# Performance work log

Measured on AMD Instinct MI355X. Metric: run time of the kernel, lower is better.

The kernel has to match this reference:

```python
import jax, jax.numpy as jnp
import numpy as np

NUM_HEADS = 8
TOPK = 16


def setup_inputs() -> dict:
    key = jax.random.key(0)
    ks = jax.random.split(key, 13)
    B, C, H, W = 2, 512, 64, 64
    Hu, Wu = H // 2, W // 2
    hd = C // NUM_HEADS
    n = lambda k, shape, s=1.0: jax.random.normal(k, shape, dtype=jnp.float32) * s
    return {
        "x": n(ks[0], (B, C, H, W)),
        "upper_feat": n(ks[1], (B, C, Hu, Wu)),
        "gumbel": jax.random.gumbel(ks[2], (B, NUM_HEADS, Hu * Wu), dtype=jnp.float32),
        # 1x1 convs (Conv2d + folded eval-mode BN => weight matrix + bias)
        "q_w": n(ks[3], (C, C), 0.02), "q_b": n(ks[4], (C,), 0.02),
        "kv_w": n(ks[5], (2 * C, C), 0.02), "kv_b": n(ks[6], (2 * C,), 0.02),
        "proj_w": n(ks[7], (C, C), 0.02), "proj_b": n(ks[8], (C,), 0.02),
        # depthwise 7x7 PE conv (groups = C)
        "pe_w": n(ks[9], (C, 1, 7, 7), 0.02), "pe_b": n(ks[10], (C,), 0.02),
        # gate conv1d kernel_size=1: [head_dim, 2*head_dim]
        "gate_w": n(ks[11], (hd, 2 * hd), 0.02), "gate_b": n(ks[12], (hd,), 0.02),
    }


def reference(x, upper_feat, gumbel, q_w, q_b, kv_w, kv_b, proj_w, proj_b,
              pe_w, pe_b, gate_w, gate_b):
    B, C, H, W = x.shape
    hd = C // NUM_HEADS
    Hu, Wu = upper_feat.shape[2], upper_feat.shape[3]
    N, Nu = H * W, Hu * Wu
    scale = hd ** -0.5

    def conv1x1(t, w, b):
        return jnp.einsum('bchw,oc->bohw', t, w) + b[None, :, None, None]

    # coarse attention: q from x, k/v from upper_feat
    q = conv1x1(x, q_w, q_b).reshape(B, NUM_HEADS, hd, N).transpose(0, 1, 3, 2)          # [B,h,N,d]
    kv = conv1x1(upper_feat, kv_w, kv_b).reshape(B, NUM_HEADS, 2 * hd, Nu).transpose(0, 1, 3, 2)
    k, v = kv[..., :hd], kv[..., hd:]                                                    # [B,h,Nu,d]
    sim = jnp.einsum('bhnd,bhmd->bhnm', q, k) * scale                                    # [B,h,N,Nu]
    attn = jax.nn.softmax(sim, axis=-1)
    coarse = jnp.einsum('bhnm,bhmd->bhnd', attn, v)                                      # [B,h,N,d]

    # fine branch: kv from x, top-k token selection via gumbel-softmax scores
    f_kv = conv1x1(x, kv_w, kv_b).reshape(B, NUM_HEADS, 2 * hd, N).transpose(0, 1, 3, 2)
    f_k, f_v = f_kv[..., :hd], f_kv[..., hd:]                                            # [B,h,N,d]

    # heat: channel-mean of x, adaptive-avg-pooled 2x2 to upper resolution (no grad)
    heat = jax.lax.stop_gradient(
        x.mean(axis=1).reshape(B, Hu, 2, Wu, 2).mean(axis=(2, 4)).reshape(B, Nu))
    global_sim = sim.mean(axis=2) * heat[:, None, :]                                     # [B,h,Nu]
    soft_weights = jax.nn.softmax(global_sim + gumbel, axis=-1)
    _, idx = jax.lax.top_k(soft_weights, TOPK)                                           # [B,h,K]

    # map each selected upper-token to its 2x2 block of x-tokens
    h_idx = (idx // Wu) * 2
    w_idx = (idx % Wu) * 2
    idx_full = jnp.concatenate(
        [(h_idx + dh) * W + (w_idx + dw) for dh in range(2) for dw in range(2)], axis=-1)  # [B,h,4K]

    topk_k = jnp.take_along_axis(f_k, idx_full[..., None], axis=2)                       # [B,h,4K,d]
    topk_v = jnp.take_along_axis(f_v, idx_full[..., None], axis=2)
    fine = jax.nn.softmax(jnp.einsum('bhnd,bhmd->bhnm', q, topk_k) * scale, axis=-1)
    refined = jnp.einsum('bhnm,bhmd->bhnd', fine, topk_v)                                # [B,h,N,d]

    # gated fusion (conv1d kernel_size=1 == per-token linear over 2d channels)
    fusion = jnp.concatenate([coarse, refined], axis=-1)                                 # [B,h,N,2d]
    gate = jax.nn.sigmoid(jnp.einsum('bhnc,oc->bhno', fusion, gate_w) + gate_b)
    out = gate * refined + (1.0 - gate) * coarse                                         # [B,h,N,d]

    x_out = out.transpose(0, 1, 3, 2).reshape(B, C, H, W)

    # positional encoding: depthwise 7x7 conv on v, bilinear upsample to (H,W)
    v_rs = v.transpose(0, 1, 3, 2).reshape(B, C, Hu, Wu)
    v_pe = jax.lax.conv_general_dilated(
        v_rs, pe_w, (1, 1), ((3, 3), (3, 3)), feature_group_count=C,
        dimension_numbers=('NCHW', 'OIHW', 'NCHW')) + pe_b[None, :, None, None]
    v_pe = jax.image.resize(v_pe, (B, C, H, W), method='bilinear')

    return conv1x1(x_out + v_pe, proj_w, proj_b)
```

## Files before the change

kernel.cpp:

```cpp
#include <hip/hip_runtime.h>
#include <hip/hip_bf16.h>
#include <cstdint>

typedef __hip_bfloat16 bf16;
typedef unsigned short u16;
typedef __attribute__((ext_vector_type(8))) short bf16x8;
typedef __attribute__((ext_vector_type(4))) float f32x4;

static __device__ __forceinline__ float bs2f(u16 s) {
  unsigned int u = ((unsigned int)s) << 16;
  float f;
  __builtin_memcpy(&f, &u, 4);
  return f;
}
static __device__ __forceinline__ u16 f2bs(float f) {
  bf16 h = __float2bfloat16(f);
  u16 s;
  __builtin_memcpy(&s, &h, 2);
  return s;
}
static __device__ __forceinline__ float ldf(const void* p, size_t i, int f32) {
  return f32 ? ((const float*)p)[i] : bs2f(((const u16*)p)[i]);
}

// ... 75 lines not shown
  const int f32 = *dtf;
  const int b = blockIdx.z, m0 = blockIdx.x * 128, oo0 = blockIdx.y * 64;
  const int t = threadIdx.x, w = t >> 6, lane = t & 63;
  const int quad = lane >> 4, c = lane & 15;
  __shared__ __align__(16) u16 As[128][72];
  __shared__ __align__(16) u16 Ws[64][72];
  f32x4 acc[2][4];
#pragma unroll
  for (int nt = 0; nt < 2; ++nt)
#pragma unroll
    for (int ot = 0; ot < 4; ++ot) acc[nt][ot] = (f32x4){0.f, 0.f, 0.f, 0.f};
  const u16* Ab = A + (size_t)b * M * 512;
  const int arow = t >> 1, acol = (t & 1) * 32;
  const int wrow = t >> 2, wcol = (t & 3) * 16;

  for (int k0 = 0; k0 < 512; k0 += 64) {
    __syncthreads();
    {
      const u16* ga = Ab + (size_t)(m0 + arow) * 512 + k0 + acol;
      uint4* ad = reinterpret_cast<uint4*>(&As[arow][acol]);
      const uint4* gs = reinterpret_cast<const uint4*>(ga);
      ad[0] = gs[0]; ad[1] = gs[1]; ad[2] = gs[2]; ad[3] = gs[3];
      if (f32) {
        const float* gw = (const float*)W + (size_t)(oo0 + wrow) * 512 + k0 + wcol;
#pragma unroll
        for (int e = 0; e < 16; ++e) Ws[wrow][wcol + e] = f2bs(gw[e]);
      } else {
        const u16* gw = (const u16*)W + (size_t)(oo0 + wrow) * 512 + k0 + wcol;
        *reinterpret_cast<uint4*>(&Ws[wrow][wcol])     = *reinterpret_cast<const uint4*>(gw);
        *reinterpret_cast<uint4*>(&Ws[wrow][wcol + 8]) = *reinterpret_cast<const uint4*>(gw + 8);
      }
    }
    __syncthreads();
#pragma unroll
    for (int ks = 0; ks < 2; ++ks) {
      bf16x8 av[2];
      av[0] = *reinterpret_cast<const bf16x8*>(&As[w * 32 + c][ks * 32 + quad * 8]);
      av[1] = *reinterpret_cast<const bf16x8*>(&As[w * 32 + 16 + c][ks * 32 + quad * 8]);
#pragma unroll
      for (int ot = 0; ot < 4; ++ot) {
        bf16x8 wv = *reinterpret_cast<const bf16x8*>(&Ws[ot * 16 + c][ks * 32 + quad * 8]);
#pragma unroll
        for (int nt = 0; nt < 2; ++nt) {
          if (MODE == 3)
            acc[nt][ot] = __builtin_amdgcn_mfma_f32_16x16x32_bf16(wv, av[nt], acc[nt][ot], 0, 0, 0);
          else
            acc[nt][ot] = __builtin_amdgcn_mfma_f32_16x16x32_bf16(av[nt], wv, acc[nt][ot], 0, 0, 0);
        }
      }
    }
  }

  if (MODE == 0) {
    const int h = oo0 >> 6, bh = b * 8 + h;
#pragma unroll
    for (int ot = 0; ot < 4; ++ot) {
      int o = oo0 + ot * 16 + c;
      int d = o & 63;
      float bv = ldf(bias, o, f32);
      float qs = 0.f;
#pragma unroll
      for (int nt = 0; nt < 2; ++nt)
#pragma unroll
        for (int r = 0; r < 4; ++r) {
          int m = m0 + w * 32 + nt * 16 + quad * 4 + r;
          u16 val = f2bs(acc[nt][ot][r] + bv);
          o0[((size_t)bh * M + m) * 64 + d] = val;
          qs += bs2f(val);
        }
      qs += __shfl_xor(qs, 16, 64);
      qs += __shfl_xor(qs, 32, 64);
      if (quad == 0) atomicAdd(&qsum[bh * 64 + d], qs);
    }
  } else {
#pragma unroll
    for (int ot = 0; ot < 4; ++ot)
#pragma unroll
      for (int r = 0; r < 4; ++r) {
        int o = oo0 + ot * 16 + quad * 4 + r;
        float bv = ldf(bias, o, f32);
#pragma unroll
        for (int nt = 0; nt < 2; ++nt) {
          int m = m0 + w * 32 + nt * 16 + c;
          float val = acc[nt][ot][r] + bv;
          size_t oi_ = ((size_t)(b * 512 + o)) * M + m;
          if (f32) ((float*)ob)[oi_] = val;
          else     ((u16*)ob)[oi_] = f2bs(val);
        }
      }
  }
}

__global__ __launch_bounds__(256) void gemm_kv(
    const u16* __restrict__ A, const void* __restrict__ W,
    const void* __restrict__ bias, u16* __restrict__ kb, u16* __restrict__ vTb,
    int M, const int* __restrict__ dtf) {
  const int f32 = *dtf;
  const int b = blockIdx.z, m0 = blockIdx.x * 64, oo0 = blockIdx.y * 64;
  const int t = threadIdx.x, w = t >> 6, lane = t & 63;
  const int quad = lane >> 4, c = lane & 15;
  __shared__ __align__(16) u16 As[64][72];
  __shared__ __align__(16) u16 Ws[64][72];
  f32x4 acc[4];
#pragma unroll
  for (int ot = 0; ot < 4; ++ot) acc[ot] = (f32x4){0.f, 0.f, 0.f, 0.f};
  const u16* Ab = A + (size_t)b * M * 512;
  const int srow = t >> 2, scol = (t & 3) * 16;

  for (int k0 = 0; k0 < 512; k0 += 64) {
    __syncthreads();
    {
      const u16* ga = Ab + (size_t)(m0 + srow) * 512 + k0 + scol;
      *reinterpret_cast<uint4*>(&As[srow][scol])     = *reinterpret_cast<const uint4*>(ga);
      *reinterpret_cast<uint4*>(&As[srow][scol + 8]) = *reinterpret_cast<const uint4*>(ga + 8);
      if (f32) {
        const float* gw = (const float*)W + (size_t)(oo0 + srow) * 512 + k0 + scol;
#pragma unroll
        for (int e = 0; e < 16; ++e) Ws[srow][scol + e] = f2bs(gw[e]);
      } else {
        const u16* gw = (const u16*)W + (size_t)(oo0 + srow) * 512 + k0 + scol;
        *reinterpret_cast<uint4*>(&Ws[srow][scol])     = *reinterpret_cast<const uint4*>(gw);
        *reinterpret_cast<uint4*>(&Ws[srow][scol + 8]) = *reinterpret_cast<const uint4*>(gw + 8);
      }
    }
    __syncthreads();
#pragma unroll
    for (int ks = 0; ks < 2; ++ks) {
      bf16x8 av = *reinterpret_cast<const bf16x8*>(&As[w * 16 + c][ks * 32 + quad * 8]);
#pragma unroll
      for (int ot = 0; ot < 4; ++ot) {
        bf16x8 wv = *reinterpret_cast<const bf16x8*>(&Ws[ot * 16 + c][ks * 32 + quad * 8]);
        acc[ot] = __builtin_amdgcn_mfma_f32_16x16x32_bf16(av, wv, acc[ot], 0, 0, 0);
      }
    }
  }

#pragma unroll
  for (int ot = 0; ot < 4; ++ot) {
    int o = oo0 + ot * 16 + c;
    float bv = ldf(bias, o, f32);
    int hh = o >> 7, jj = o & 127;
#pragma unroll
    for (int r = 0; r < 4; ++r) {
      int m = m0 + w * 16 + quad * 4 + r;
      u16 val = f2bs(acc[ot][r] + bv);
      if (jj < 64) kb[((size_t)(b * 8 + hh) * M + m) * 64 + jj] = val;
      else         vTb[((size_t)(b * 8 + hh) * 64 + (jj & 63)) * M + m] = val;
    }
  }
}

__global__ __launch_bounds__(256) void topk_kernel(
    const float* __restrict__ qsum, const u16* __restrict__ k,
    const float* __restrict__ heat, const void* __restrict__ gumbel,
    int* __restrict__ posb, const int* __restrict__ dtf) {
  const int f32 = *dtf;
  int bh = blockIdx.x, b = bh >> 3, t = threadIdx.x;
  __shared__ float qs[64];
  __shared__ float s[1024];
  __shared__ float rv[256];
  __shared__ int   ri[256];
  if (t < 64) qs[t] = qsum[bh * 64 + t];
  __syncthreads();
  for (int j = 0; j < 4; ++j) {
    int m = t + j * 256;
    const u16* kr = k + ((size_t)bh * 1024 + m) * 64;
    float dot = 0.f;
    for (int d = 0; d < 64; ++d) dot += qs[d] * bs2f(kr[d]);
    s[m] = dot * (0.125f / 4096.0f) * (heat[b * 1024 + m] * (1.0f / 2048.0f)) +
           ldf(gumbel, (size_t)bh * 1024 + m, f32);
  }
  __syncthreads();
  for (int it = 0; it < 16; ++it) {
    float bv = -1e30f; int bi = 0x7fffffff;
    for (int j = 0; j < 4; ++j) {
      int m = t + j * 256; float vv = s[m];
      if (vv > bv || (vv == bv && m < bi)) { bv = vv; bi = m; }
    }
    rv[t] = bv; ri[t] = bi; __syncthreads();
    for (int off = 128; off; off >>= 1) {
      if (t < off) {
        if (rv[t + off] > rv[t] || (rv[t + off] == rv[t] && ri[t + off] < ri[t])) {
          rv[t] = rv[t + off]; ri[t] = ri[t + off];
        }
      }
      __syncthreads();
    }
    if (t == 0) {
      int mi = ri[0]; s[mi] = -1e30f;
      int hy = (mi >> 5) * 2, wx = (mi & 31) * 2;
      posb[bh * 64 + it]      = hy * 64 + wx;
      posb[bh * 64 + 16 + it] = hy * 64 + wx + 1;
      posb[bh * 64 + 32 + it] = (hy + 1) * 64 + wx;
      posb[bh * 64 + 48 + it] = (hy + 1) * 64 + wx + 1;
    }
    __syncthreads();
  }
}

__global__ __launch_bounds__(256) void gather_kv_mfma(
    const u16* __restrict__ xT, const void* __restrict__ kv_w,
    const void* __restrict__ kv_b, const int* __restrict__ posb,
    u16* __restrict__ tkb, u16* __restrict__ tvTb,
    const int* __restrict__ dtf) {
  const int f32 = *dtf;
  const int bh = blockIdx.x, b = bh >> 3, h = bh & 7;
  const int half = blockIdx.y;
  const int t = threadIdx.x, w = t >> 6, lane = t & 63;
  const int quad = lane >> 4, c = lane & 15;
  __shared__ int pos[64];
  __shared__ __align__(16) u16 As[64][72];
  __shared__ __align__(16) u16 Ws[64][72];
  if (t < 64) pos[t] = posb[bh * 64 + t];
  __syncthreads();
  const int obase = h * 128 + half * 64;
  const int srow = t >> 2, scol = (t & 3) * 16;
  const int arow = pos[srow];
  f32x4 acc[4];
#pragma unroll
  for (int ot = 0; ot < 4; ++ot) acc[ot] = (f32x4){0.f, 0.f, 0.f, 0.f};

  for (int k0 = 0; k0 < 512; k0 += 64) {
    __syncthreads();
    {
      const u16* ga = xT + ((size_t)b * 4096 + arow) * 512 + k0 + scol;
      *reinterpret_cast<uint4*>(&As[srow][scol])     = *reinterpret_cast<const uint4*>(ga);
      *reinterpret_cast<uint4*>(&As[srow][scol + 8]) = *reinterpret_cast<const uint4*>(ga + 8);
      if (f32) {
        const float* gw = (const float*)kv_w + (size_t)(obase + srow) * 512 + k0 + scol;
#pragma unroll
        for (int e = 0; e < 16; ++e) Ws[srow][scol + e] = f2bs(gw[e]);
      } else {
        const u16* gw = (const u16*)kv_w + (size_t)(obase + srow) * 512 + k0 + scol;
        *reinterpret_cast<uint4*>(&Ws[srow][scol])     = *reinterpret_cast<const uint4*>(gw);
        *reinterpret_cast<uint4*>(&Ws[srow][scol + 8]) = *reinterpret_cast<const uint4*>(gw + 8);
      }
    }
    __syncthreads();
#pragma unroll
    for (int ks = 0; ks < 2; ++ks) {
      bf16x8 av = *reinterpret_cast<const bf16x8*>(&As[w * 16 + c][ks * 32 + quad * 8]);
#pragma unroll
      for (int ot = 0; ot < 4; ++ot) {
        bf16x8 wv = *reinterpret_cast<const bf16x8*>(&Ws[ot * 16 + c][ks * 32 + quad * 8]);
        acc[ot] = __builtin_amdgcn_mfma_f32_16x16x32_bf16(av, wv, acc[ot], 0, 0, 0);
      }
    }
  }

#pragma unroll
  for (int ot = 0; ot < 4; ++ot) {
    int d = ot * 16 + c;
    float bv = ldf(kv_b, obase + d, f32);
#pragma unroll
    for (int r = 0; r < 4; ++r) {
      int m = w * 16 + quad * 4 + r;
      u16 val = f2bs(acc[ot][r] + bv);
      if (half) tvTb[((size_t)bh * 64 + d) * 64 + m] = val;
      else      tkb[((size_t)bh * 64 + m) * 64 + d] = val;
    }
  }
}

__global__ __launch_bounds__(256) void dwconv_kernel(
    const u16* __restrict__ vT, const void* __restrict__ pe_w,
    const void* __restrict__ pe_b, u16* __restrict__ vpe,
    const int* __restrict__ dtf) {
  const int f32 = *dtf;
  int bc = blockIdx.x;
  int b = bc >> 9, c = bc & 511;
  int h = c >> 6, d = c & 63;
  int t = threadIdx.x;
  __shared__ float img[1024];
  __shared__ float wts[49];
  const u16* base = vT + ((size_t)(b * 8 + h) * 64 + d) * 1024;
  if (t < 128) {
    uint4 v4 = reinterpret_cast<const uint4*>(base)[t];
    u16 tmp[8];
    *reinterpret_cast<uint4*>(tmp) = v4;
#pragma unroll
    for (int e = 0; e < 8; ++e) img[t * 8 + e] = bs2f(tmp[e]);
  }
  if (t < 49) wts[t] = ldf(pe_w, c * 49 + t, f32);
  float bias = ldf(pe_b, c, f32);
  __syncthreads();
  for (int i = t; i < 1024; i += 256) {
    int y = i >> 5, xx = i & 31;
    float a = 0.f;
#pragma unroll
    for (int ky = 0; ky < 7; ++ky) {
      int yy = y + ky - 3;
      if ((unsigned)yy >= 32u) continue;
#pragma unroll
      for (int kx = 0; kx < 7; ++kx) {
        int xc = xx + kx - 3;
        if ((unsigned)xc >= 32u) continue;
        a += img[yy * 32 + xc] * wts[ky * 7 + kx];
      }
    }
    vpe[(size_t)bc * 1024 + i] = f2bs(a + bias);
  }
}

__global__ __launch_bounds__(256) void attn_fused(
    const u16* __restrict__ q, const u16* __restrict__ k,
    const u16* __restrict__ vT, const u16* __restrict__ tkb,
    const u16* __restrict__ tvTb, const u16* __restrict__ gwb,
    const float* __restrict__ gbf, const u16* __restrict__ vpe,
    u16* __restrict__ xsT) {
  const int bh = blockIdx.y, b = bh >> 3, h = bh & 7;
  const int bx = blockIdx.x;
  const int n0 = bx * 128;
  const int t = threadIdx.x, w = t >> 6, lane = t & 63;
  const int quad = lane >> 4, c = lane & 15;

  __shared__ __align__(16) u16 lds[27648];
  u16* Ks = lds;
  u16* Vt = lds + 9216;
  u16* Ps = lds + 18432;

  bf16x8 bq[2][2];
#pragma unroll
  for (int nt = 0; nt < 2; ++nt) {
    const u16* qr = q + ((size_t)bh * 4096 + n0 + w * 32 + nt * 16 + c) * 64;
    bq[nt][0] = *reinterpret_cast<const bf16x8*>(qr + quad * 8);
    bq[nt][1] = *reinterpret_cast<const bf16x8*>(qr + 32 + quad * 8);
  }
  f32x4 po[2][4];
#pragma unroll
  for (int nt = 0; nt < 2; ++nt)
#pragma unroll
    for (int dt = 0; dt < 4; ++dt) po[nt][dt] = (f32x4){0.f, 0.f, 0.f, 0.f};
  float sume[2] = {0.f, 0.f};

  const u16* kbase = k + (size_t)bh * 65536;
  const u16* vbase = vT + (size_t)bh * 65536;
  const int srow = t >> 2, scol = (t & 3) * 16;

  uint4 kr0, kr1, vr0, vr1;
  {
    const u16* gk = kbase + (size_t)srow * 64 + scol;
    kr0 = *reinterpret_cast<const uint4*>(gk);
    kr1 = *reinterpret_cast<const uint4*>(gk + 8);
    const u16* gv = vbase + (size_t)srow * 1024 + scol;
    vr0 = *reinterpret_cast<const uint4*>(gv);
    vr1 = *reinterpret_cast<const uint4*>(gv + 8);
    *reinterpret_cast<uint4*>(&Ks[srow * 72 + scol])     = kr0;
    *reinterpret_cast<uint4*>(&Ks[srow * 72 + scol + 8]) = kr1;
    *reinterpret_cast<uint4*>(&Vt[srow * 72 + scol])     = vr0;
    *reinterpret_cast<uint4*>(&Vt[srow * 72 + scol + 8]) = vr1;
  }

  for (int ch = 0; ch < 16; ++ch) {
    __syncthreads();
    const int buf = ch & 1;
    if (ch + 1 < 16) {
      int m1 = (ch + 1) * 64;
      const u16* gk = kbase + (size_t)(m1 + srow) * 64 + scol;
      kr0 = *reinterpret_cast<const uint4*>(gk);
      kr1 = *reinterpret_cast<const uint4*>(gk + 8);
      const u16* gv = vbase + (size_t)srow * 1024 + m1 + scol;
      vr0 = *reinterpret_cast<const uint4*>(gv);
      vr1 = *reinterpret_cast<const uint4*>(gv + 8);
    }

    f32x4 st[2][4];
#pragma unroll
    for (int mt = 0; mt < 4; ++mt) {
      const u16* krow = &Ks[(buf * 64 + mt * 16 + c) * 72];
      bf16x8 ak0 = *reinterpret_cast<const bf16x8*>(krow + quad * 8);
      bf16x8 ak1 = *reinterpret_cast<const bf16x8*>(krow + 32 + quad * 8);
#pragma unroll
      for (int nt = 0; nt < 2; ++nt) {
        f32x4 acc = (f32x4){0.f, 0.f, 0.f, 0.f};
        acc = __builtin_amdgcn_mfma_f32_16x16x32_bf16(ak0, bq[nt][0], acc, 0, 0, 0);
        acc = __builtin_amdgcn_mfma_f32_16x16x32_bf16(ak1, bq[nt][1], acc, 0, 0, 0);
        st[nt][mt] = acc;
      }
    }
#pragma unroll
    for (int nt = 0; nt < 2; ++nt) {
      float cs = 0.f;
      u16* psw = &Ps[((w * 2 + nt) * 16 + c) * 72];
#pragma unroll
      for (int mt = 0; mt < 4; ++mt) {
        float e0 = __expf(st[nt][mt][0] * 0.125f);
        float e1 = __expf(st[nt][mt][1] * 0.125f);
        float e2 = __expf(st[nt][mt][2] * 0.125f);
        float e3 = __expf(st[nt][mt][3] * 0.125f);
        cs += (e0 + e1) + (e2 + e3);
        ushort4 pw;
        pw.x = f2bs(e0); pw.y = f2bs(e1); pw.z = f2bs(e2); pw.w = f2bs(e3);
        *reinterpret_cast<ushort4*>(psw + mt * 16 + quad * 4) = pw;
      }
      cs += __shfl_xor(cs, 16, 64);
      cs += __shfl_xor(cs, 32, 64);
      sume[nt] += cs;
    }
#pragma unroll
    for (int s = 0; s < 2; ++s) {
      bf16x8 bp0 = *reinterpret_cast<const bf16x8*>(&Ps[((w * 2 + 0) * 16 + c) * 72 + s * 32 + quad * 8]);
      bf16x8 bp1 = *reinterpret_cast<const bf16x8*>(&Ps[((w * 2 + 1) * 16 + c) * 72 + s * 32 + quad * 8]);
#pragma unroll
      for (int dt = 0; dt < 4; ++dt) {
        bf16x8 av = *reinterpret_cast<const bf16x8*>(&Vt[(buf * 64 + dt * 16 + c) * 72 + s * 32 + quad * 8]);
        po[0][dt] = __builtin_amdgcn_mfma_f32_16x16x32_bf16(av, bp0, po[0][dt], 0, 0, 0);
        po[1][dt] = __builtin_amdgcn_mfma_f32_16x16x32_bf16(av, bp1, po[1][dt], 0, 0, 0);
      }
    }

    if (ch + 1 < 16) {
      const int nb = buf ^ 1;
      *reinterpret_cast<uint4*>(&Ks[(nb * 64 + srow) * 72 + scol])     = kr0;
      *reinterpret_cast<uint4*>(&Ks[(nb * 64 + srow) * 72 + scol + 8]) = kr1;
      *reinterpret_cast<uint4*>(&Vt[(nb * 64 + srow) * 72 + scol])     = vr0;
      *reinterpret_cast<uint4*>(&Vt[(nb * 64 + srow) * 72 + scol + 8]) = vr1;
    }
  }

  __syncthreads();
  u16* fus = lds;
  u16* vl  = lds + 17408;
  float* gbl = (float*)(lds + 25088);

  for (int idx = t; idx < 768; idx += 256) {
    int seg = idx & 3, ch2 = (idx >> 2) & 63, r = idx >> 8;
    int vrow = bx - 1 + r;
    vrow = vrow < 0 ? 0 : (vrow > 31 ? 31 : vrow);
    const uint4* src = reinterpret_cast<const uint4*>(
        vpe + ((size_t)(b * 512 + h * 64 + ch2)) * 1024 + vrow * 32);
    *reinterpret_cast<uint4*>(&vl[(r * 64 + ch2) * 40 + seg * 8]) = src[seg];
  }
  if (t < 64) gbl[t] = gbf[t];
  __syncthreads();

  for (int nt = 0; nt < 2; ++nt) {
    u16* fusw = &fus[((w * 2 + nt) * 16 + c) * 136];
    f32x4 st[4];
#pragma unroll
    for (int mt = 0; mt < 4; ++mt) {
      f32x4 acc = (f32x4){0.f, 0.f, 0.f, 0.f};
#pragma unroll
      for (int s = 0; s < 2; ++s) {
        bf16x8 ak = *reinterpret_cast<const bf16x8*>(
            &tkb[((size_t)bh * 64 + mt * 16 + c) * 64 + s * 32 + quad * 8]);
        acc = __builtin_amdgcn_mfma_f32_16x16x32_bf16(ak, bq[nt][s], acc, 0, 0, 0);
      }
      st[mt] = acc;
    }
    float sume2 = 0.f;
#pragma unroll
    for (int mt = 0; mt < 4; ++mt) {
      float e0 = __expf(st[mt][0] * 0.125f);
      float e1 = __expf(st[mt][1] * 0.125f);
      float e2 = __expf(st[mt][2] * 0.125f);
      float e3 = __expf(st[mt][3] * 0.125f);
      sume2 += (e0 + e1) + (e2 + e3);
      ushort4 pw;
      pw.x = f2bs(e0); pw.y = f2bs(e1); pw.z = f2bs(e2); pw.w = f2bs(e3);
      *reinterpret_cast<ushort4*>(fusw + mt * 16 + quad * 4) = pw;
    }
    sume2 += __shfl_xor(sume2, 16, 64);
    sume2 += __shfl_xor(sume2, 32, 64);
    float inv2 = 1.0f / sume2;

    f32x4 po2[4];
#pragma unroll
    for (int dt = 0; dt < 4; ++dt) po2[dt] = (f32x4){0.f, 0.f, 0.f, 0.f};
#pragma unroll
    for (int s = 0; s < 2; ++s) {
      bf16x8 bp = *reinterpret_cast<const bf16x8*>(fusw + s * 32 + quad * 8);
#pragma unroll
      for (int dt = 0; dt < 4; ++dt) {
        bf16x8 av = *reinterpret_cast<const bf16x8*>(
            &tvTb[((size_t)bh * 64 + dt * 16 + c) * 64 + s * 32 + quad * 8]);
        po2[dt] = __builtin_amdgcn_mfma_f32_16x16x32_bf16(av, bp, po2[dt], 0, 0, 0);
      }
    }

    float invc = 1.0f / sume[nt];
#pragma unroll
    for (int dt = 0; dt < 4; ++dt) {
      ushort4 cw, rw;
      cw.x = f2bs(po[nt][dt][0] * invc); cw.y = f2bs(po[nt][dt][1] * invc);
      cw.z = f2bs(po[nt][dt][2] * invc); cw.w = f2bs(po[nt][dt][3] * invc);
      rw.x = f2bs(po2[dt][0] * inv2);    rw.y = f2bs(po2[dt][1] * inv2);
      rw.z = f2bs(po2[dt][2] * inv2);    rw.w = f2bs(po2[dt][3] * inv2);
      *reinterpret_cast<ushort4*>(fusw + dt * 16 + quad * 4)      = cw;
      *reinterpret_cast<ushort4*>(fusw + 64 + dt * 16 + quad * 4) = rw;
    }

    f32x4 ga[4];
#pragma unroll
    for (int ot = 0; ot < 4; ++ot) ga[ot] = (f32x4){0.f, 0.f, 0.f, 0.f};
#pragma unroll
    for (int s = 0; s < 4; ++s) {
      bf16x8 bf = *reinterpret_cast<const bf16x8*>(fusw + s * 32 + quad * 8);
#pragma unroll
      for (int ot = 0; ot < 4; ++ot) {
        bf16x8 ag = *reinterpret_cast<const bf16x8*>(
            gwb + (ot * 16 + c) * 128 + s * 32 + quad * 8);
        ga[ot] = __builtin_amdgcn_mfma_f32_16x16x32_bf16(ag, bf, ga[ot], 0, 0, 0);
      }
    }

    const int ylocal = (w * 32 + nt * 16) >> 6;
    const int x = (w * 32 + nt * 16 + c) & 63;
    float wy0, wy1; int i0, i1;
    if (ylocal == 0) { wy0 = 0.25f; wy1 = 0.75f; i0 = (bx > 0) ? 0 : 1; i1 = 1; }
    else             { wy0 = 0.75f; wy1 = 0.25f; i0 = 1; i1 = (bx < 31) ? 2 : 1; }
    int jx = x >> 1, x0, x1; float wx0, wx1;
    if ((x & 1) == 0) { x0 = (jx > 0) ? jx - 1 : 0; x1 = jx; wx0 = 0.25f; wx1 = 0.75f; }
    else              { x0 = jx; x1 = (jx < 31) ? jx + 1 : 31; wx0 = 0.75f; wx1 = 0.25f; }
#pragma unroll
    for (int dt = 0; dt < 4; ++dt) {
      ushort4 ow;
      u16 tmp[4];
#pragma unroll
      for (int r = 0; r < 4; ++r) {
        int row = dt * 16 + quad * 4 + r;
        float ref = po2[dt][r] * inv2;
        float coar = bs2f(fusw[row]);
        float g = 1.0f / (1.0f + __expf(-(ga[dt][r] + gbl[row])));
        float vv = wy0 * (wx0 * bs2f(vl[(i0 * 64 + row) * 40 + x0]) +
                          wx1 * bs2f(vl[(i0 * 64 + row) * 40 + x1])) +
                   wy1 * (wx0 * bs2f(vl[(i1 * 64 + row) * 40 + x0]) +
                          wx1 * bs2f(vl[(i1 * 64 + row) * 40 + x1]));
        tmp[r] = f2bs(g * ref + (1.0f - g) * coar + vv);
      }
      ow.x = tmp[0]; ow.y = tmp[1]; ow.z = tmp[2]; ow.w = tmp[3];
      *reinterpret_cast<ushort4*>(fusw + dt * 16 + quad * 4) = ow;
    }

    {
      int nl = lane >> 2, cs = (lane & 3) * 16;
      const u16* srcrow = &fus[((w * 2 + nt) * 16 + nl) * 136 + cs];
      u16* dst = xsT + ((size_t)b * 4096 + n0 + w * 32 + nt * 16 + nl) * 512 + h * 64 + cs;
      *reinterpret_cast<uint4*>(dst)     = *reinterpret_cast<const uint4*>(srcrow);
      *reinterpret_cast<uint4*>(dst + 8) = *reinterpret_cast<const uint4*>(srcrow + 8);
    }
  }
}

extern "C" void kernel_launch(void* const* d_in, const int* in_sizes, int n_in,
                              void* d_out, int out_size, void* d_ws, size_t ws_size,
                              hipStream_t stream) {
  const void* x    = d_in[0];
  const void* up   = d_in[1];
  const void* gum  = d_in[2];
  const void* q_w  = d_in[3];
  const void* q_b  = d_in[4];
  const void* kv_w = d_in[5];
  const void* kv_b = d_in[6];
  const void* p_w  = d_in[7];
  const void* p_b  = d_in[8];
  const void* pe_w = d_in[9];
  const void* pe_b = d_in[10];
  const void* g_w  = d_in[11];
  const void* g_b  = d_in[12];

  float* ws    = (float*)d_ws;
  int*   dtf   = (int*)ws;
  float* qsum  = ws + 16;
  float* heat  = qsum + 1024;
  int*   posb  = (int*)(heat + 2048);
  float* gbf   = (float*)(posb + 1024);
  u16*   gwb   = (u16*)(gbf + 64);
  u16*   tkb   = gwb + 8192;
  u16*   tvTb  = tkb + 65536;
  u16*   qb    = tvTb + 65536;
  u16*   kb    = qb + 4194304;
  u16*   vTb   = kb + 1048576;
  u16*   xT    = vTb + 1048576;
  u16*   upT   = xT + 4194304;
  u16*   xsT   = upT + 1048576;
  u16*   vpe   = xsT + 4194304;

  dim3 blk(256);
  hipMemsetAsync(ws, 0, (16 + 1024 + 2048) * 4, stream);
  detect_dtype<<<dim3(64), blk, 0, stream>>>((const uint4*)x, dtf);
  prep_gate<<<dim3(1), blk, 0, stream>>>(g_w, g_b, gwb, gbf, dtf);
  transpose_bf16<<<dim3(64, 8, 2), blk, 0, stream>>>(x, xT, 4096, heat, dtf);
  transpose_bf16<<<dim3(16, 8, 2), blk, 0, stream>>>(up, upT, 1024, nullptr, dtf);
  gemm128<0><<<dim3(32, 8, 2), blk, 0, stream>>>(xT, q_w, q_b, qb, nullptr, qsum, 4096, dtf);
  gemm_kv<<<dim3(16, 16, 2), blk, 0, stream>>>(upT, kv_w, kv_b, kb, vTb, 1024, dtf);
  topk_kernel<<<dim3(16), blk, 0, stream>>>(qsum, kb, heat, gum, posb, dtf);
  gather_kv_mfma<<<dim3(16, 2), blk, 0, stream>>>(xT, kv_w, kv_b, posb, tkb, tvTb, dtf);
  dwconv_kernel<<<dim3(1024), blk, 0, stream>>>(vTb, pe_w, pe_b, vpe, dtf);
  attn_fused<<<dim3(32, 16), blk, 0, stream>>>(qb, kb, vTb, tkb, tvTb, gwb, gbf, vpe, xsT);
  gemm128<3><<<dim3(32, 8, 2), blk, 0, stream>>>(xsT, p_w, p_b, nullptr, d_out, nullptr, 4096, dtf);
}
```

Baseline: 261.7 us.

## Halve attention tile to 64 queries per block and single-buffer K/V

The fused attention kernel now handles 64 query tokens per block instead of 128, one 16-row tile per wave, and the grid doubles to 64x16 blocks. K/V chunks move from a double-buffered LDS ring to a single buffer with an extra barrier per chunk, which halves LDS use and adds a launch-bounds occupancy hint. The aim is more resident blocks and waves per CU to hide latency on 1024 blocks. The costs are re-reading all of K/V once per smaller block and more synchronization stalls, since the prefetched K/V chunk no longer overlaps the MFMA work.

```diff
diff --git a/kernel.cpp b/kernel.cpp
--- a/kernel.cpp
+++ b/kernel.cpp
@@ -401,7 +401,7 @@
   }
 }
 
-__global__ __launch_bounds__(256) void attn_fused(
+__global__ __launch_bounds__(256, 4) void attn_fused(
     const u16* __restrict__ q, const u16* __restrict__ k,
     const u16* __restrict__ vT, const u16* __restrict__ tkb,
     const u16* __restrict__ tvTb, const u16* __restrict__ gwb,
@@ -409,28 +409,25 @@
     u16* __restrict__ xsT) {
   const int bh = blockIdx.y, b = bh >> 3, h = bh & 7;
   const int bx = blockIdx.x;
-  const int n0 = bx * 128;
+  const int n0 = bx * 64;
   const int t = threadIdx.x, w = t >> 6, lane = t & 63;
   const int quad = lane >> 4, c = lane & 15;
 
-  __shared__ __align__(16) u16 lds[27648];
+  __shared__ __align__(16) u16 lds[13824];
   u16* Ks = lds;
-  u16* Vt = lds + 9216;
-  u16* Ps = lds + 18432;
-
-  bf16x8 bq[2][2];
-#pragma unroll
-  for (int nt = 0; nt < 2; ++nt) {
-    const u16* qr = q + ((size_t)bh * 4096 + n0 + w * 32 + nt * 16 + c) * 64;
-    bq[nt][0] = *reinterpret_cast<const bf16x8*>(qr + quad * 8);
-    bq[nt][1] = *reinterpret_cast<const bf16x8*>(qr + 32 + quad * 8);
-  }
-  f32x4 po[2][4];
-#pragma unroll
-  for (int nt = 0; nt < 2; ++nt)
-#pragma unroll
-    for (int dt = 0; dt < 4; ++dt) po[nt][dt] = (f32x4){0.f, 0.f, 0.f, 0.f};
-  float sume[2] = {0.f, 0.f};
+  u16* Vt = lds + 4608;
+  u16* Ps = lds + 9216;
+
+  bf16x8 bq[2];
+  {
+    const u16* qr = q + ((size_t)bh * 4096 + n0 + w * 16 + c) * 64;
+    bq[0] = *reinterpret_cast<const bf16x8*>(qr + quad * 8);
+    bq[1] = *reinterpret_cast<const bf16x8*>(qr + 32 + quad * 8);
+  }
+  f32x4 po[4];
+#pragma unroll
+  for (int dt = 0; dt < 4; ++dt) po[dt] = (f32x4){0.f, 0.f, 0.f, 0.f};
+  float sume = 0.f;
 
   const u16* kbase = k + (size_t)bh * 65536;
   const u16* vbase = vT + (size_t)bh * 65536;
@@ -444,17 +441,17 @@
     const u16* gv = vbase + (size_t)srow * 1024 + scol;
     vr0 = *reinterpret_cast<const uint4*>(gv);
     vr1 = *reinterpret_cast<const uint4*>(gv + 8);
+  }
+
+  for (int ch = 0; ch < 16; ++ch) {
+    __syncthreads();
     *reinterpret_cast<uint4*>(&Ks[srow * 72 + scol])     = kr0;
     *reinterpret_cast<uint4*>(&Ks[srow * 72 + scol + 8]) = kr1;
     *reinterpret_cast<uint4*>(&Vt[srow * 72 + scol])     = vr0;
     *reinterpret_cast<uint4*>(&Vt[srow * 72 + scol + 8]) = vr1;
-  }
-
-  for (int ch = 0; ch < 16; ++ch) {
-    __syncthreads();
-    const int buf = ch & 1;
+    __syncthreads();
     if (ch + 1 < 16) {
-      int m1 = (ch + 1) * 64;
+      const int m1 = (ch + 1) * 64;
       const u16* gk = kbase + (size_t)(m1 + srow) * 64 + scol;
       kr0 = *reinterpret_cast<const uint4*>(gk);
       kr1 = *reinterpret_cast<const uint4*>(gk + 8);
@@ -463,181 +460,167 @@
       vr1 = *reinterpret_cast<const uint4*>(gv + 8);
     }
 
-    f32x4 st[2][4];
+    f32x4 st[4];
 #pragma unroll
     for (int mt = 0; mt < 4; ++mt) {
-      const u16* krow = &Ks[(buf * 64 + mt * 16 + c) * 72];
+      const u16* krow = &Ks[(mt * 16 + c) * 72];
       bf16x8 ak0 = *reinterpret_cast<const bf16x8*>(krow + quad * 8);
       bf16x8 ak1 = *reinterpret_cast<const bf16x8*>(krow + 32 + quad * 8);
-#pragma unroll
-      for (int nt = 0; nt < 2; ++nt) {
-        f32x4 acc = (f32x4){0.f, 0.f, 0.f, 0.f};
-        acc = __builtin_amdgcn_mfma_f32_16x16x32_bf16(ak0, bq[nt][0], acc, 0, 0, 0);
-        acc = __builtin_amdgcn_mfma_f32_16x16x32_bf16(ak1, bq[nt][1], acc, 0, 0, 0);
-        st[nt][mt] = acc;
-      }
-    }
-#pragma unroll
-    for (int nt = 0; nt < 2; ++nt) {
-      float cs = 0.f;
-      u16* psw = &Ps[((w * 2 + nt) * 16 + c) * 72];
-#pragma unroll
-      for (int mt = 0; mt < 4; ++mt) {
-        float e0 = __expf(st[nt][mt][0] * 0.125f);
-        float e1 = __expf(st[nt][mt][1] * 0.125f);
-        float e2 = __expf(st[nt][mt][2] * 0.125f);
-        float e3 = __expf(st[nt][mt][3] * 0.125f);
-        cs += (e0 + e1) + (e2 + e3);
-        ushort4 pw;
-        pw.x = f2bs(e0); pw.y = f2bs(e1); pw.z = f2bs(e2); pw.w = f2bs(e3);
-        *reinterpret_cast<ushort4*>(psw + mt * 16 + quad * 4) = pw;
-      }
-      cs += __shfl_xor(cs, 16, 64);
-      cs += __shfl_xor(cs, 32, 64);
-      sume[nt] += cs;
-    }
-#pragma unroll
-    for (int s = 0; s < 2; ++s) {
-      bf16x8 bp0 = *reinterpret_cast<const bf16x8*>(&Ps[((w * 2 + 0) * 16 + c) * 72 + s * 32 + quad * 8]);
-      bf16x8 bp1 = *reinterpret_cast<const bf16x8*>(&Ps[((w * 2 + 1) * 16 + c) * 72 + s * 32 + quad * 8]);
-#pragma unroll
-      for (int dt = 0; dt < 4; ++dt) {
-        bf16x8 av = *reinterpret_cast<const bf16x8*>(&Vt[(buf * 64 + dt * 16 + c) * 72 + s * 32 + quad * 8]);
-        po[0][dt] = __builtin_amdgcn_mfma_f32_16x16x32_bf16(av, bp0, po[0][dt], 0, 0, 0);
-        po[1][dt] = __builtin_amdgcn_mfma_f32_16x16x32_bf16(av, bp1, po[1][dt], 0, 0, 0);
-      }
-    }
-
-    if (ch + 1 < 16) {
-      const int nb = buf ^ 1;
-      *reinterpret_cast<uint4*>(&Ks[(nb * 64 + srow) * 72 + scol])     = kr0;
-      *reinterpret_cast<uint4*>(&Ks[(nb * 64 + srow) * 72 + scol + 8]) = kr1;
-      *reinterpret_cast<uint4*>(&Vt[(nb * 64 + srow) * 72 + scol])     = vr0;
-      *reinterpret_cast<uint4*>(&Vt[(nb * 64 + srow) * 72 + scol + 8]) = vr1;
-    }
-  }
-
-  __syncthreads();
-  u16* fus = lds;
-  u16* vl  = lds + 17408;
-  float* gbl = (float*)(lds + 25088);
-
-  for (int idx = t; idx < 768; idx += 256) {
-    int seg = idx & 3, ch2 = (idx >> 2) & 63, r = idx >> 8;
-    int vrow = bx - 1 + r;
-    vrow = vrow < 0 ? 0 : (vrow > 31 ? 31 : vrow);
-    const uint4* src = reinterpret_cast<const uint4*>(
-        vpe + ((size_t)(b * 512 + h * 64 + ch2)) * 1024 + vrow * 32);
-    *reinterpret_cast<uint4*>(&vl[(r * 64 + ch2) * 40 + seg * 8]) = src[seg];
-  }
-  if (t < 64) gbl[t] = gbf[t];
-  __syncthreads();
-
-  for (int nt = 0; nt < 2; ++nt) {
-    u16* fusw = &fus[((w * 2 + nt) * 16 + c) * 136];
-    f32x4 st[4];
-#pragma unroll
-    for (int mt = 0; mt < 4; ++mt) {
       f32x4 acc = (f32x4){0.f, 0.f, 0.f, 0.f};
-#pragma unroll
-      for (int s = 0; s < 2; ++s) {
-        bf16x8 ak = *reinterpret_cast<const bf16x8*>(
-            &tkb[((size_t)bh * 64 + mt * 16 + c) * 64 + s * 32 + quad * 8]);
-        acc = __builtin_amdgcn_mfma_f32_16x16x32_bf16(ak, bq[nt][s], acc, 0, 0, 0);
-      }
+      acc = __builtin_amdgcn_mfma_f32_16x16x32_bf16(ak0, bq[0], acc, 0, 0, 0);
+      acc = __builtin_amdgcn_mfma_f32_16x16x32_bf16(ak1, bq[1], acc, 0, 0, 0);
       st[mt] = acc;
     }
-    float sume2 = 0.f;
+    float cs = 0.f;
+    u16* psw = &Ps[(w * 16 + c) * 72];
 #pragma unroll
     for (int mt = 0; mt < 4; ++mt) {
       float e0 = __expf(st[mt][0] * 0.125f);
       float e1 = __expf(st[mt][1] * 0.125f);
       float e2 = __expf(st[mt][2] * 0.125f);
       float e3 = __expf(st[mt][3] * 0.125f);
-      sume2 += (e0 + e1) + (e2 + e3);
+      cs += (e0 + e1) + (e2 + e3);
       ushort4 pw;
       pw.x = f2bs(e0); pw.y = f2bs(e1); pw.z = f2bs(e2); pw.w = f2bs(e3);
-      *reinterpret_cast<ushort4*>(fusw + mt * 16 + quad * 4) = pw;
-    }
-    sume2 += __shfl_xor(sume2, 16, 64);
-    sume2 += __shfl_xor(sume2, 32, 64);
-    float inv2 = 1.0f / sume2;
-
-    f32x4 po2[4];
-#pragma unroll
-    for (int dt = 0; dt < 4; ++dt) po2[dt] = (f32x4){0.f, 0.f, 0.f, 0.f};
+      *reinterpret_cast<ushort4*>(psw + mt * 16 + quad * 4) = pw;
+    }
+    cs += __shfl_xor(cs, 16, 64);
+    cs += __shfl_xor(cs, 32, 64);
+    sume += cs;
 #pragma unroll
     for (int s = 0; s < 2; ++s) {
-      bf16x8 bp = *reinterpret_cast<const bf16x8*>(fusw + s * 32 + quad * 8);
+      bf16x8 bp = *reinterpret_cast<const bf16x8*>(psw + s * 32 + quad * 8);
 #pragma unroll
       for (int dt = 0; dt < 4; ++dt) {
-        bf16x8 av = *reinterpret_cast<const bf16x8*>(
-            &tvTb[((size_t)bh * 64 + dt * 16 + c) * 64 + s * 32 + quad * 8]);
-        po2[dt] = __builtin_amdgcn_mfma_f32_16x16x32_bf16(av, bp, po2[dt], 0, 0, 0);
-      }
-    }
-
-    float invc = 1.0f / sume[nt];
+        bf16x8 av = *reinterpret_cast<const bf16x8*>(&Vt[(dt * 16 + c) * 72 + s * 32 + quad * 8]);
+        po[dt] = __builtin_amdgcn_mfma_f32_16x16x32_bf16(av, bp, po[dt], 0, 0, 0);
+      }
+    }
+  }
+
+  __syncthreads();
+  u16* fus = lds;
+  u16* vl  = lds + 8704;
+  float* gbl = (float*)(lds + 13312);
+
+  const int ym = bx >> 1;
+  int r0_, r1_; float wy0, wy1;
+  if ((bx & 1) == 0) { r0_ = ym > 0 ? ym - 1 : 0; r1_ = ym; wy0 = 0.25f; wy1 = 0.75f; }
+  else               { r0_ = ym; r1_ = ym < 31 ? ym + 1 : 31; wy0 = 0.75f; wy1 = 0.25f; }
+
+  for (int idx = t; idx < 512; idx += 256) {
+    int seg = idx & 3, ch2 = (idx >> 2) & 63, rr = idx >> 8;
+    int vrow = rr ? r1_ : r0_;
+    const uint4 v4 = *reinterpret_cast<const uint4*>(
+        vpe + ((size_t)(b * 512 + h * 64 + ch2)) * 1024 + vrow * 32 + seg * 8);
+    u16* dst = &vl[(rr * 64 + ch2) * 36 + seg * 8];
+    uint2 lo, hi;
+    lo.x = v4.x; lo.y = v4.y; hi.x = v4.z; hi.y = v4.w;
+    *reinterpret_cast<uint2*>(dst)     = lo;
+    *reinterpret_cast<uint2*>(dst + 4) = hi;
+  }
+  if (t < 64) gbl[t] = gbf[t];
+  __syncthreads();
+
+  u16* fusw = &fus[(w * 16 + c) * 136];
+  f32x4 st2[4];
+#pragma unroll
+  for (int mt = 0; mt < 4; ++mt) {
+    f32x4 acc = (f32x4){0.f, 0.f, 0.f, 0.f};
+#pragma unroll
+    for (int s = 0; s < 2; ++s) {
+      bf16x8 ak = *reinterpret_cast<const bf16x8*>(
+          &tkb[((size_t)bh * 64 + mt * 16 + c) * 64 + s * 32 + quad * 8]);
+      acc = __builtin_amdgcn_mfma_f32_16x16x32_bf16(ak, bq[s], acc, 0, 0, 0);
+    }
+    st2[mt] = acc;
+  }
+  float sume2 = 0.f;
+#pragma unroll
+  for (int mt = 0; mt < 4; ++mt) {
+    float e0 = __expf(st2[mt][0] * 0.125f);
+    float e1 = __expf(st2[mt][1] * 0.125f);
+    float e2 = __expf(st2[mt][2] * 0.125f);
+    float e3 = __expf(st2[mt][3] * 0.125f);
+    sume2 += (e0 + e1) + (e2 + e3);
+    ushort4 pw;
+    pw.x = f2bs(e0); pw.y = f2bs(e1); pw.z = f2bs(e2); pw.w = f2bs(e3);
+    *reinterpret_cast<ushort4*>(fusw + mt * 16 + quad * 4) = pw;
+  }
+  sume2 += __shfl_xor(sume2, 16, 64);
+  sume2 += __shfl_xor(sume2, 32, 64);
+  float inv2 = 1.0f / sume2;
+
+  f32x4 po2[4];
+#pragma unroll
+  for (int dt = 0; dt < 4; ++dt) po2[dt] = (f32x4){0.f, 0.f, 0.f, 0.f};
+#pragma unroll
+  for (int s = 0; s < 2; ++s) {
+    bf16x8 bp = *reinterpret_cast<const bf16x8*>(fusw + s * 32 + quad * 8);
 #pragma unroll
     for (int dt = 0; dt < 4; ++dt) {
-      ushort4 cw, rw;
-      cw.x = f2bs(po[nt][dt][0] * invc); cw.y = f2bs(po[nt][dt][1] * invc);
-      cw.z = f2bs(po[nt][dt][2] * invc); cw.w = f2bs(po[nt][dt][3] * invc);
-      rw.x = f2bs(po2[dt][0] * inv2);    rw.y = f2bs(po2[dt][1] * inv2);
-      rw.z = f2bs(po2[dt][2] * inv2);    rw.w = f2bs(po2[dt][3] * inv2);
-      *reinterpret_cast<ushort4*>(fusw + dt * 16 + quad * 4)      = cw;
-      *reinterpret_cast<ushort4*>(fusw + 64 + dt * 16 + quad * 4) = rw;
-    }
-
-    f32x4 ga[4];
-#pragma unroll
-    for (int ot = 0; ot < 4; ++ot) ga[ot] = (f32x4){0.f, 0.f, 0.f, 0.f};
-#pragma unroll
-    for (int s = 0; s < 4; ++s) {
-      bf16x8 bf = *reinterpret_cast<const bf16x8*>(fusw + s * 32 + quad * 8);
-#pragma unroll
-      for (int ot = 0; ot < 4; ++ot) {
-        bf16x8 ag = *reinterpret_cast<const bf16x8*>(
-            gwb + (ot * 16 + c) * 128 + s * 32 + quad * 8);
-        ga[ot] = __builtin_amdgcn_mfma_f32_16x16x32_bf16(ag, bf, ga[ot], 0, 0, 0);
-      }
-    }
-
-    const int ylocal = (w * 32 + nt * 16) >> 6;
-    const int x = (w * 32 + nt * 16 + c) & 63;
-    float wy0, wy1; int i0, i1;
-    if (ylocal == 0) { wy0 = 0.25f; wy1 = 0.75f; i0 = (bx > 0) ? 0 : 1; i1 = 1; }
-    else             { wy0 = 0.75f; wy1 = 0.25f; i0 = 1; i1 = (bx < 31) ? 2 : 1; }
-    int jx = x >> 1, x0, x1; float wx0, wx1;
-    if ((x & 1) == 0) { x0 = (jx > 0) ? jx - 1 : 0; x1 = jx; wx0 = 0.25f; wx1 = 0.75f; }
-    else              { x0 = jx; x1 = (jx < 31) ? jx + 1 : 31; wx0 = 0.75f; wx1 = 0.25f; }
-#pragma unroll
-    for (int dt = 0; dt < 4; ++dt) {
-      ushort4 ow;
-      u16 tmp[4];
-#pragma unroll
-      for (int r = 0; r < 4; ++r) {
-        int row = dt * 16 + quad * 4 + r;
-        float ref = po2[dt][r] * inv2;
-        float coar = bs2f(fusw[row]);
-        float g = 1.0f / (1.0f + __expf(-(ga[dt][r] + gbl[row])));
-        float vv = wy0 * (wx0 * bs2f(vl[(i0 * 64 + row) * 40 + x0]) +
-                          wx1 * bs2f(vl[(i0 * 64 + row) * 40 + x1])) +
-                   wy1 * (wx0 * bs2f(vl[(i1 * 64 + row) * 40 + x0]) +
-                          wx1 * bs2f(vl[(i1 * 64 + row) * 40 + x1]));
-        tmp[r] = f2bs(g * ref + (1.0f - g) * coar + vv);
-      }
-      ow.x = tmp[0]; ow.y = tmp[1]; ow.z = tmp[2]; ow.w = tmp[3];
-      *reinterpret_cast<ushort4*>(fusw + dt * 16 + quad * 4) = ow;
-    }
-
-    {
-      int nl = lane >> 2, cs = (lane & 3) * 16;
-      const u16* srcrow = &fus[((w * 2 + nt) * 16 + nl) * 136 + cs];
-      u16* dst = xsT + ((size_t)b * 4096 + n0 + w * 32 + nt * 16 + nl) * 512 + h * 64 + cs;
-      *reinterpret_cast<uint4*>(dst)     = *reinterpret_cast<const uint4*>(srcrow);
-      *reinterpret_cast<uint4*>(dst + 8) = *reinterpret_cast<const uint4*>(srcrow + 8);
-    }
+      bf16x8 av = *reinterpret_cast<const bf16x8*>(
+          &tvTb[((size_t)bh * 64 + dt * 16 + c) * 64 + s * 32 + quad * 8]);
+      po2[dt] = __builtin_amdgcn_mfma_f32_16x16x32_bf16(av, bp, po2[dt], 0, 0, 0);
+    }
+  }
+
+  float invc = 1.0f / sume;
+#pragma unroll
+  for (int dt = 0; dt < 4; ++dt) {
+    ushort4 cw, rw;
+    cw.x = f2bs(po[dt][0] * invc); cw.y = f2bs(po[dt][1] * invc);
+    cw.z = f2bs(po[dt][2] * invc); cw.w = f2bs(po[dt][3] * invc);
+    rw.x = f2bs(po2[dt][0] * inv2); rw.y = f2bs(po2[dt][1] * inv2);
+    rw.z = f2bs(po2[dt][2] * inv2); rw.w = f2bs(po2[dt][3] * inv2);
+    *reinterpret_cast<ushort4*>(fusw + dt * 16 + quad * 4)      = cw;
+    *reinterpret_cast<ushort4*>(fusw + 64 + dt * 16 + quad * 4) = rw;
+  }
+
+  f32x4 ga[4];
+#pragma unroll
+  for (int ot = 0; ot < 4; ++ot) ga[ot] = (f32x4){0.f, 0.f, 0.f, 0.f};
+#pragma unroll
+  for (int s = 0; s < 4; ++s) {
+    bf16x8 bf = *reinterpret_cast<const bf16x8*>(fusw + s * 32 + quad * 8);
+#pragma unroll
+    for (int ot = 0; ot < 4; ++ot) {
+      bf16x8 ag = *reinterpret_cast<const bf16x8*>(
+          gwb + (ot * 16 + c) * 128 + s * 32 + quad * 8);
+      ga[ot] = __builtin_amdgcn_mfma_f32_16x16x32_bf16(ag, bf, ga[ot], 0, 0, 0);
+    }
+  }
+
+  const int x = w * 16 + c;
+  int jx = x >> 1, x0, x1; float wx0, wx1;
+  if ((x & 1) == 0) { x0 = (jx > 0) ? jx - 1 : 0; x1 = jx; wx0 = 0.25f; wx1 = 0.75f; }
+  else              { x0 = jx; x1 = (jx < 31) ? jx + 1 : 31; wx0 = 0.75f; wx1 = 0.25f; }
+#pragma unroll
+  for (int dt = 0; dt < 4; ++dt) {
+    ushort4 ow;
+    u16 tmp[4];
+#pragma unroll
+    for (int r = 0; r < 4; ++r) {
+      int row = dt * 16 + quad * 4 + r;
+      float ref = po2[dt][r] * inv2;
+      float coar = bs2f(fusw[row]);
+      float g = 1.0f / (1.0f + __expf(-(ga[dt][r] + gbl[row])));
+      float vv = wy0 * (wx0 * bs2f(vl[row * 36 + x0]) +
+                        wx1 * bs2f(vl[row * 36 + x1])) +
+                 wy1 * (wx0 * bs2f(vl[(64 + row) * 36 + x0]) +
+                        wx1 * bs2f(vl[(64 + row) * 36 + x1]));
+      tmp[r] = f2bs(g * ref + (1.0f - g) * coar + vv);
+    }
+    ow.x = tmp[0]; ow.y = tmp[1]; ow.z = tmp[2]; ow.w = tmp[3];
+    *reinterpret_cast<ushort4*>(fusw + dt * 16 + quad * 4) = ow;
+  }
+
+  {
+    int nl = lane >> 2, cs2 = (lane & 3) * 16;
+    const u16* srcrow = &fus[(w * 16 + nl) * 136 + cs2];
+    u16* dst = xsT + ((size_t)b * 4096 + n0 + w * 16 + nl) * 512 + h * 64 + cs2;
+    *reinterpret_cast<uint4*>(dst)     = *reinterpret_cast<const uint4*>(srcrow);
+    *reinterpret_cast<uint4*>(dst + 8) = *reinterpret_cast<const uint4*>(srcrow + 8);
   }
 }
 
@@ -686,6 +669,6 @@
   topk_kernel<<<dim3(16), blk, 0, stream>>>(qsum, kb, heat, gum, posb, dtf);
   gather_kv_mfma<<<dim3(16, 2), blk, 0, stream>>>(xT, kv_w, kv_b, posb, tkb, tvTb, dtf);
   dwconv_kernel<<<dim3(1024), blk, 0, stream>>>(vTb, pe_w, pe_b, vpe, dtf);
-  attn_fused<<<dim3(32, 16), blk, 0, stream>>>(qb, kb, vTb, tkb, tvTb, gwb, gbf, vpe, xsT);
+  attn_fused<<<dim3(64, 16), blk, 0, stream>>>(qb, kb, vTb, tkb, tvTb, gwb, gbf, vpe, xsT);
   gemm128<3><<<dim3(32, 8, 2), blk, 0, stream>>>(xsT, p_w, p_b, nullptr, d_out, nullptr, 4096, dtf);
 }
```

New measurement: 262.5 us. No clear change (+0.3%).

## Single-buffer K/V tiles and shrink LDS to raise attention kernel occupancy

Applied to the files above, without the earlier changes.

Removes the double-buffered K/V staging in the coarse attention loop. Each chunk now goes into a single LDS buffer between two barriers, with the next chunk still prefetched into registers. The fusion scratch is reused per wave instead of per n-tile, and the vpe tile stride drops from 40 to 36. Together these cut shared memory from about 54KB to 36KB, and launch bounds now request 4 blocks per CU. The aim is higher occupancy to hide latency, at the cost of an extra barrier per chunk and possible register pressure.

```diff
diff --git a/kernel.cpp b/kernel.cpp
--- a/kernel.cpp
+++ b/kernel.cpp
@@ -401,7 +401,7 @@
   }
 }
 
-__global__ __launch_bounds__(256) void attn_fused(
+__global__ __launch_bounds__(256, 4) void attn_fused(
     const u16* __restrict__ q, const u16* __restrict__ k,
     const u16* __restrict__ vT, const u16* __restrict__ tkb,
     const u16* __restrict__ tvTb, const u16* __restrict__ gwb,
@@ -413,10 +413,10 @@
   const int t = threadIdx.x, w = t >> 6, lane = t & 63;
   const int quad = lane >> 4, c = lane & 15;
 
-  __shared__ __align__(16) u16 lds[27648];
+  __shared__ __align__(16) u16 lds[18432];
   u16* Ks = lds;
-  u16* Vt = lds + 9216;
-  u16* Ps = lds + 18432;
+  u16* Vt = lds + 4608;
+  u16* Ps = lds + 9216;
 
   bf16x8 bq[2][2];
 #pragma unroll
@@ -444,17 +444,17 @@
     const u16* gv = vbase + (size_t)srow * 1024 + scol;
     vr0 = *reinterpret_cast<const uint4*>(gv);
     vr1 = *reinterpret_cast<const uint4*>(gv + 8);
+  }
+
+  for (int ch = 0; ch < 16; ++ch) {
+    __syncthreads();
     *reinterpret_cast<uint4*>(&Ks[srow * 72 + scol])     = kr0;
     *reinterpret_cast<uint4*>(&Ks[srow * 72 + scol + 8]) = kr1;
     *reinterpret_cast<uint4*>(&Vt[srow * 72 + scol])     = vr0;
     *reinterpret_cast<uint4*>(&Vt[srow * 72 + scol + 8]) = vr1;
-  }
-
-  for (int ch = 0; ch < 16; ++ch) {
-    __syncthreads();
-    const int buf = ch & 1;
+    __syncthreads();
     if (ch + 1 < 16) {
-      int m1 = (ch + 1) * 64;
+      const int m1 = (ch + 1) * 64;
       const u16* gk = kbase + (size_t)(m1 + srow) * 64 + scol;
       kr0 = *reinterpret_cast<const uint4*>(gk);
       kr1 = *reinterpret_cast<const uint4*>(gk + 8);
@@ -466,7 +466,7 @@
     f32x4 st[2][4];
 #pragma unroll
     for (int mt = 0; mt < 4; ++mt) {
-      const u16* krow = &Ks[(buf * 64 + mt * 16 + c) * 72];
+      const u16* krow = &Ks[(mt * 16 + c) * 72];
       bf16x8 ak0 = *reinterpret_cast<const bf16x8*>(krow + quad * 8);
       bf16x8 ak1 = *reinterpret_cast<const bf16x8*>(krow + 32 + quad * 8);
 #pragma unroll
@@ -502,40 +502,36 @@
       bf16x8 bp1 = *reinterpret_cast<const bf16x8*>(&Ps[((w * 2 + 1) * 16 + c) * 72 + s * 32 + quad * 8]);
 #pragma unroll
       for (int dt = 0; dt < 4; ++dt) {
-        bf16x8 av = *reinterpret_cast<const bf16x8*>(&Vt[(buf * 64 + dt * 16 + c) * 72 + s * 32 + quad * 8]);
+        bf16x8 av = *reinterpret_cast<const bf16x8*>(&Vt[(dt * 16 + c) * 72 + s * 32 + quad * 8]);
         po[0][dt] = __builtin_amdgcn_mfma_f32_16x16x32_bf16(av, bp0, po[0][dt], 0, 0, 0);
         po[1][dt] = __builtin_amdgcn_mfma_f32_16x16x32_bf16(av, bp1, po[1][dt], 0, 0, 0);
       }
     }
-
-    if (ch + 1 < 16) {
-      const int nb = buf ^ 1;
-      *reinterpret_cast<uint4*>(&Ks[(nb * 64 + srow) * 72 + scol])     = kr0;
-      *reinterpret_cast<uint4*>(&Ks[(nb * 64 + srow) * 72 + scol + 8]) = kr1;
-      *reinterpret_cast<uint4*>(&Vt[(nb * 64 + srow) * 72 + scol])     = vr0;
-      *reinterpret_cast<uint4*>(&Vt[(nb * 64 + srow) * 72 + scol + 8]) = vr1;
-    }
   }
 
   __syncthreads();
   u16* fus = lds;
-  u16* vl  = lds + 17408;
-  float* gbl = (float*)(lds + 25088);
+  u16* vl  = lds + 8704;
+  float* gbl = (float*)(lds + 15616);
 
   for (int idx = t; idx < 768; idx += 256) {
-    int seg = idx & 3, ch2 = (idx >> 2) & 63, r = idx >> 8;
-    int vrow = bx - 1 + r;
+    int seg = idx & 3, ch2 = (idx >> 2) & 63, rr = idx >> 8;
+    int vrow = bx - 1 + rr;
     vrow = vrow < 0 ? 0 : (vrow > 31 ? 31 : vrow);
-    const uint4* src = reinterpret_cast<const uint4*>(
-        vpe + ((size_t)(b * 512 + h * 64 + ch2)) * 1024 + vrow * 32);
-    *reinterpret_cast<uint4*>(&vl[(r * 64 + ch2) * 40 + seg * 8]) = src[seg];
+    const uint4 v4 = *reinterpret_cast<const uint4*>(
+        vpe + ((size_t)(b * 512 + h * 64 + ch2)) * 1024 + vrow * 32 + seg * 8);
+    u16* dst = &vl[(rr * 64 + ch2) * 36 + seg * 8];
+    uint2 lo, hi;
+    lo.x = v4.x; lo.y = v4.y; hi.x = v4.z; hi.y = v4.w;
+    *reinterpret_cast<uint2*>(dst)     = lo;
+    *reinterpret_cast<uint2*>(dst + 4) = hi;
   }
   if (t < 64) gbl[t] = gbf[t];
   __syncthreads();
 
   for (int nt = 0; nt < 2; ++nt) {
-    u16* fusw = &fus[((w * 2 + nt) * 16 + c) * 136];
-    f32x4 st[4];
+    u16* fusw = &fus[(w * 16 + c) * 136];
+    f32x4 st2[4];
 #pragma unroll
     for (int mt = 0; mt < 4; ++mt) {
       f32x4 acc = (f32x4){0.f, 0.f, 0.f, 0.f};
@@ -545,15 +541,15 @@
             &tkb[((size_t)bh * 64 + mt * 16 + c) * 64 + s * 32 + quad * 8]);
         acc = __builtin_amdgcn_mfma_f32_16x16x32_bf16(ak, bq[nt][s], acc, 0, 0, 0);
       }
-      st[mt] = acc;
+      st2[mt] = acc;
     }
     float sume2 = 0.f;
 #pragma unroll
     for (int mt = 0; mt < 4; ++mt) {
-      float e0 = __expf(st[mt][0] * 0.125f);
-      float e1 = __expf(st[mt][1] * 0.125f);
-      float e2 = __expf(st[mt][2] * 0.125f);
-      float e3 = __expf(st[mt][3] * 0.125f);
+      float e0 = __expf(st2[mt][0] * 0.125f);
+      float e1 = __expf(st2[mt][1] * 0.125f);
+      float e2 = __expf(st2[mt][2] * 0.125f);
+      float e3 = __expf(st2[mt][3] * 0.125f);
       sume2 += (e0 + e1) + (e2 + e3);
       ushort4 pw;
       pw.x = f2bs(e0); pw.y = f2bs(e1); pw.z = f2bs(e2); pw.w = f2bs(e3);
@@ -621,10 +617,10 @@
         float ref = po2[dt][r] * inv2;
         float coar = bs2f(fusw[row]);
         float g = 1.0f / (1.0f + __expf(-(ga[dt][r] + gbl[row])));
-        float vv = wy0 * (wx0 * bs2f(vl[(i0 * 64 + row) * 40 + x0]) +
-                          wx1 * bs2f(vl[(i0 * 64 + row) * 40 + x1])) +
-                   wy1 * (wx0 * bs2f(vl[(i1 * 64 + row) * 40 + x0]) +
-                          wx1 * bs2f(vl[(i1 * 64 + row) * 40 + x1]));
+        float vv = wy0 * (wx0 * bs2f(vl[(i0 * 64 + row) * 36 + x0]) +
+                          wx1 * bs2f(vl[(i0 * 64 + row) * 36 + x1])) +
+                   wy1 * (wx0 * bs2f(vl[(i1 * 64 + row) * 36 + x0]) +
+                          wx1 * bs2f(vl[(i1 * 64 + row) * 36 + x1]));
         tmp[r] = f2bs(g * ref + (1.0f - g) * coar + vv);
       }
       ow.x = tmp[0]; ow.y = tmp[1]; ow.z = tmp[2]; ow.w = tmp[3];
@@ -632,9 +628,9 @@
     }
 
     {
-      int nl = lane >> 2, cs = (lane & 3) * 16;
-      const u16* srcrow = &fus[((w * 2 + nt) * 16 + nl) * 136 + cs];
-      u16* dst = xsT + ((size_t)b * 4096 + n0 + w * 32 + nt * 16 + nl) * 512 + h * 64 + cs;
+      int nl = lane >> 2, cs2 = (lane & 3) * 16;
+      const u16* srcrow = &fus[(w * 16 + nl) * 136 + cs2];
+      u16* dst = xsT + ((size_t)b * 4096 + n0 + w * 32 + nt * 16 + nl) * 512 + h * 64 + cs2;
       *reinterpret_cast<uint4*>(dst)     = *reinterpret_cast<const uint4*>(srcrow);
       *reinterpret_cast<uint4*>(dst + 8) = *reinterpret_cast<const uint4*>(srcrow + 8);
     }
```

New measurement: 277.2 us. 5.9% more time.
